# Performance work log

Hardware: AMD Instinct MI355X
Metric: run time of the kernel (lower is better)

The kernel has to match this reference:

```python
import jax, jax.numpy as jnp
import numpy as np

H = 12      # heads
P = 4       # dim_point
CHUNK = 256 # chunk_size
DIM_SINGLE = 768
DIM_PAIR = 64
B, N = 1, 1024


def setup_inputs() -> dict:
    key = jax.random.key(0)
    ks = jax.random.split(key, 24)
    s = 0.02
    d = DIM_SINGLE
    inp = {
        'single': jax.random.normal(ks[0], (B, N, d), jnp.float32),
        'pair': jax.random.normal(ks[1], (B, N, N, DIM_PAIR), jnp.float32),
        'rot': jax.random.normal(ks[2], (B, N, 3, 3), jnp.float32),
        'trans': jax.random.normal(ks[3], (B, N, 3), jnp.float32),
        # Linear weights stored as (in, out) so y = x @ W + b
        'Wq': jax.random.normal(ks[4], (d, d), jnp.float32) * s,
        'bq': jnp.zeros((d,), jnp.float32),
        'Wk': jax.random.normal(ks[5], (d, d), jnp.float32) * s,
        'bk': jnp.zeros((d,), jnp.float32),
        'Wv': jax.random.normal(ks[6], (d, d), jnp.float32) * s,
        'bv': jnp.zeros((d,), jnp.float32),
        'Wpb': jax.random.normal(ks[7], (DIM_PAIR, H), jnp.float32) * s,
        'bpb': jnp.zeros((H,), jnp.float32),
        'Wqp': jax.random.normal(ks[8], (d, H * P * 3), jnp.float32) * s,
        'bqp': jnp.zeros((H * P * 3,), jnp.float32),
        'Wkp': jax.random.normal(ks[9], (d, H * P * 3), jnp.float32) * s,
        'bkp': jnp.zeros((H * P * 3,), jnp.float32),
        'Wvp': jax.random.normal(ks[10], (d, H * P * 3), jnp.float32) * s,
        'bvp': jnp.zeros((H * P * 3,), jnp.float32),
        'Wo': jax.random.normal(ks[11], (d, d), jnp.float32) * s,
        'bo': jnp.zeros((d,), jnp.float32),
        'Wpo': jax.random.normal(ks[12], (H * P * 3, d), jnp.float32) * s,
        'bpo': jnp.zeros((d,), jnp.float32),
        'ln_g': jnp.ones((d,), jnp.float32),
        'ln_b': jnp.zeros((d,), jnp.float32),
    }
    return inp


def _layernorm(x, g, b, eps=1e-5):
    mu = jnp.mean(x, axis=-1, keepdims=True)
    var = jnp.mean((x - mu) ** 2, axis=-1, keepdims=True)
    return (x - mu) * jax.lax.rsqrt(var + eps) * g + b


def reference(single, pair, rot, trans, Wq, bq, Wk, bk, Wv, bv, Wpb, bpb,
              Wqp, bqp, Wkp, bkp, Wvp, bvp, Wo, bo, Wpo, bpo, ln_g, ln_b):
    Bs, Ns, C = single.shape
    Ch = C // H
    scale = Ch ** (-0.5)

    q = (single @ Wq + bq).reshape(Bs, Ns, H, Ch)
    k = (single @ Wk + bk).reshape(Bs, Ns, H, Ch)
    v = (single @ Wv + bv).reshape(Bs, Ns, H, Ch)

    # [B,N,N,H] -> [B,H,N,M]
    pair_bias = jnp.transpose(pair @ Wpb + bpb, (0, 3, 1, 2))

    q_pts = (single @ Wqp + bqp).reshape(Bs, Ns, H, P, 3)
    k_pts = (single @ Wkp + bkp).reshape(Bs, Ns, H, P, 3)
    v_pts = (single @ Wvp + bvp).reshape(Bs, Ns, H, P, 3)

    t = trans[:, :, None, None, :]  # [B,N,1,1,3]
    q_pts_g = jnp.einsum('bnhpd,bnde->bnhpe', q_pts, rot) + t
    k_pts_g = jnp.einsum('bnhpd,bnde->bnhpe', k_pts, rot) + t
    v_pts_g = jnp.einsum('bnhpd,bnde->bnhpe', v_pts, rot) + t

    q2_h = jnp.transpose(jnp.sum(q_pts_g ** 2, axis=(3, 4)), (0, 2, 1))  # [B,H,N]
    k2_h = jnp.transpose(jnp.sum(k_pts_g ** 2, axis=(3, 4)), (0, 2, 1))  # [B,H,N]

    scalar_logits = jnp.einsum('bnhc,bmhc->bhnm', q, k) * scale  # [B,H,N,N]

    out_scalar = jnp.zeros((Bs, Ns, H, Ch), single.dtype)
    out_points = jnp.zeros((Bs, Ns, H, P, 3), single.dtype)

    # Faithful to the original: softmax is taken PER CHUNK over the key axis,
    # and the per-chunk weighted sums are accumulated.
    for start in range(0, Ns, CHUNK):
        end = min(start + CHUNK, Ns)
        qk = jnp.einsum('bnhpd,bmhpd->bhnm', q_pts_g, k_pts_g[:, start:end])
        pt_logits = -0.5 * (q2_h[:, :, :, None] + k2_h[:, :, None, start:end]
                            - 2.0 * qk) * scale
        logits = scalar_logits[:, :, :, start:end] + pair_bias[:, :, :, start:end] + pt_logits
        attn = jax.nn.softmax(logits, axis=-1)  # [B,H,N,chunk]
        out_scalar = out_scalar + jnp.einsum('bhnm,bmhc->bnhc', attn, v[:, start:end])
        out_points = out_points + jnp.einsum('bhnm,bmhpd->bnhpd', attn, v_pts_g[:, start:end])

    weighted_scalar = out_scalar.reshape(Bs, Ns, H * Ch)
    weighted_points = out_points.reshape(Bs, Ns, H * P * 3)
    point_proj = weighted_points @ Wpo + bpo
    out = (weighted_scalar + point_proj) @ Wo + bo
    return _layernorm(single + out, ln_g, ln_b)
```

## Files before the change

kernel.cpp:

```cpp
#include <hip/hip_runtime.h>
#include <hip/hip_bf16.h>
#include <stdint.h>

#define NTOK 1024
#define NH 12
#define QPSLAB 2801664

typedef short bf16x8 __attribute__((ext_vector_type(8)));
typedef float f32x4 __attribute__((ext_vector_type(4)));
typedef uint32_t u32x4 __attribute__((ext_vector_type(4)));

__device__ __forceinline__ unsigned short f2bf(float f) {
  union { float f; uint32_t u; } x; x.f = f;
  uint32_t r = x.u + 0x7FFFu + ((x.u >> 16) & 1u);
  return (unsigned short)(r >> 16);
}
__device__ __forceinline__ float bf2f(unsigned short u) {
  union { uint32_t u; float f; } x; x.u = ((uint32_t)u) << 16;
  return x.f;
}
__device__ __forceinline__ bf16x8 pack8(float4 a, float4 b) {
  union { __hip_bfloat162 h2[4]; bf16x8 v; } u;
  u.h2[0] = __float22bfloat162_rn(make_float2(a.x, a.y));
  u.h2[1] = __float22bfloat162_rn(make_float2(a.z, a.w));
  u.h2[2] = __float22bfloat162_rn(make_float2(b.x, b.y));
  u.h2[3] = __float22bfloat162_rn(make_float2(b.z, b.w));
  return u.v;
}

__global__ __launch_bounds__(256) void prep_k(
    const float* __restrict__ single, const float* __restrict__ Wq,
    const float* __restrict__ Wk, const float* __restrict__ Wv,
    const float* __restrict__ Wqp, const float* __restrict__ Wkp,
    const float* __restrict__ Wvp, const float* __restrict__ Wpo,
    const float* __restrict__ Wo, const float* __restrict__ Wpb,
    const float* __restrict__ bq, const float* __restrict__ bk,
    const float* __restrict__ bv, const float* __restrict__ bqp,
    const float* __restrict__ bkp, const float* __restrict__ bvp,
    unsigned short* __restrict__ sgl, unsigned short* __restrict__ wcat,
    unsigned short* __restrict__ WB, unsigned short* __restrict__ wpoA,
    float* __restrict__ bcat, unsigned short* __restrict__ wpbt)
{
  const int bid = blockIdx.x, t = threadIdx.x;
  if (bid < 2628) {
    __shared__ unsigned short tl[16][72];
    int b = bid;
    const float* src; unsigned short* dst; int N, dstld, rowbase;
    if (b < 1728) {
      int j = b / 576; b -= j * 576;
      src = (j == 0) ? Wq : (j == 1) ? Wk : Wv;
      N = 768; dst = wcat; dstld = 768; rowbase = j * 768;
    } else if (b < 2052) {
      b -= 1728; int j = b / 108; b -= j * 108;
      src = (j == 0) ? Wqp : (j == 1) ? Wkp : Wvp;
      N = 144; dst = wcat; dstld = 768; rowbase = 2304 + j * 144;
    } else {
      b -= 2052; src = Wo; N = 768; dst = WB; dstld = 912; rowbase = 0;
    }
    const int k0 = (b % 12) * 64, n0 = (b / 12) * 16;
#pragma unroll
    for (int i = 0; i < 4; ++i) {
      int kk = (t >> 4) + i * 16;
      int nn = t & 15;
      tl[nn][kk] = f2bf(src[(size_t)(k0 + kk) * N + n0 + nn]);
    }
    __syncthreads();
#pragma unroll
    for (int i = 0; i < 4; ++i) {
      int kk = t & 63;
      int nn = (t >> 6) + i * 4;
      dst[(size_t)(rowbase + n0 + nn) * dstld + k0 + kk] = tl[nn][kk];
    }
    return;
  }
  if (bid < 3396) {
    int i = (bid - 2628) * 256 + t;
    float4 v = *(const float4*)(single + (size_t)i * 4);
    ushort4 o;
    o.x = f2bf(v.x); o.y = f2bf(v.y); o.z = f2bf(v.z); o.w = f2bf(v.w);
    *(ushort4*)(sgl + (size_t)i * 4) = o;
    return;
  }
  if (bid < 3504) {
    int i = (bid - 3396) * 256 + t;
    float4 v = *(const float4*)(Wpo + (size_t)i * 4);
    ushort4 o;
    o.x = f2bf(v.x); o.y = f2bf(v.y); o.z = f2bf(v.z); o.w = f2bf(v.w);
    *(ushort4*)(wpoA + (size_t)i * 4) = o;
    return;
  }
  if (bid < 3515) {
    int idx = (bid - 3504) * 256 + t;
    if (idx < 2736) {
      float v;
      if (idx < 768) v = bq[idx];
      else if (idx < 1536) v = bk[idx - 768];
      else if (idx < 2304) v = bv[idx - 1536];
      else if (idx < 2448) v = bqp[idx - 2304];
      else if (idx < 2592) v = bkp[idx - 2448];
      else v = bvp[idx - 2592];
      bcat[idx] = v;
    }
    return;
  }
  {
    int idx = (bid - 3515) * 256 + t;
    int h = idx >> 6, k = idx & 63;
    wpbt[idx] = (h < 12) ? f2bf(Wpb[k * 12 + h]) : (unsigned short)0;
  }
}

template <int EPI>
__device__ __forceinline__ void gemm_dev(
    unsigned short* As, unsigned short* Bs,
    const unsigned short* __restrict__ A, int lda, int Mact,
    const unsigned short* __restrict__ Bt, int ldb, int Nact,
    int kt0, int ktn, int kmax,
    float* __restrict__ outf, unsigned short* __restrict__ outb, int ldc,
    const float* __restrict__ p0, int mb, int nb, int addbias)
{
  const int t = threadIdx.x;
  const int w = t >> 6, lane = t & 63;
  const int wr = w >> 1, wc = w & 1;
  const int lr = lane & 15, lc = lane >> 4;
  const int m0 = mb * 128, n0 = nb * 128;
  const int r0 = t >> 2, c0 = t & 3;
  const int r1 = r0 + 64;

  f32x4 acc[4][4] = {};
  u32x4 zz = {0u, 0u, 0u, 0u};
  u32x4 pa0, pa1, pq0, pq1;

#define LOAD_AB(KT)                                                              \
  do {                                                                           \
    int k0_ = (KT) * 32;                                                         \
    int g0_ = k0_ + c0 * 8;                                                      \
    pa0 = (g0_ < kmax && (m0 + r0) < Mact)                                       \
              ? *(const u32x4*)(A + (size_t)(m0 + r0) * lda + g0_) : zz;         \
    pa1 = (g0_ < kmax && (m0 + r1) < Mact)                                       \
              ? *(const u32x4*)(A + (size_t)(m0 + r1) * lda + g0_) : zz;         \
    pq0 = (g0_ < kmax && (n0 + r0) < Nact)                                       \
              ? *(const u32x4*)(Bt + (size_t)(n0 + r0) * ldb + g0_) : zz;        \
    pq1 = (g0_ < kmax && (n0 + r1) < Nact)                                       \
              ? *(const u32x4*)(Bt + (size_t)(n0 + r1) * ldb + g0_) : zz;        \
  } while (0)

  LOAD_AB(kt0);
  for (int kt = kt0; kt < kt0 + ktn; ++kt) {
    __syncthreads();
    ((u32x4*)As)[r0 * 4 + c0] = pa0;
    ((u32x4*)As)[r1 * 4 + c0] = pa1;
    ((u32x4*)Bs)[r0 * 4 + c0] = pq0;
    ((u32x4*)Bs)[r1 * 4 + c0] = pq1;
    __syncthreads();
    if (kt + 1 < kt0 + ktn) LOAD_AB(kt + 1);

    bf16x8 af[4], bfr[4];
#pragma unroll
    for (int mi = 0; mi < 4; ++mi) {
      int row = wr * 64 + mi * 16 + lr;
      af[mi] = *(const bf16x8*)(As + (row * 4 + lc) * 8);
    }
#pragma unroll
    for (int ni = 0; ni < 4; ++ni) {
      int row = wc * 64 + ni * 16 + lr;
      bfr[ni] = *(const bf16x8*)(Bs + (row * 4 + lc) * 8);
    }
#pragma unroll
    for (int mi = 0; mi < 4; ++mi)
#pragma unroll
      for (int ni = 0; ni < 4; ++ni)
        acc[mi][ni] = __builtin_amdgcn_mfma_f32_16x16x32_bf16(
            af[mi], bfr[ni], acc[mi][ni], 0, 0, 0);
  }
#undef LOAD_AB

#pragma unroll
  for (int mi = 0; mi < 4; ++mi) {
#pragma unroll
    for (int ni = 0; ni < 4; ++ni) {
#pragma unroll
      for (int r = 0; r < 4; ++r) {
        int row = m0 + wr * 64 + mi * 16 + lc * 4 + r;
        int col = n0 + wc * 64 + ni * 16 + lr;
        if (row < Mact && col < Nact) {
          float v = acc[mi][ni][r];
          if constexpr (EPI == 0) {
            outf[(size_t)row * ldc + col] = addbias ? (v + p0[col]) : v;
          } else {
            outb[(size_t)col * 912 + 768 + row] = f2bf(v);
          }
        }
      }
    }
  }
}

__global__ __launch_bounds__(256) void fat_k(
    const unsigned short* __restrict__ sgl, const unsigned short* __restrict__ wcat,
    const float* __restrict__ bcat, float* __restrict__ qp2,
    const float* __restrict__ pair, const unsigned short* __restrict__ wpbt,
    const float* __restrict__ bpb, unsigned short* __restrict__ pb,
    const unsigned short* __restrict__ wpoA, unsigned short* __restrict__ WB,
    const float* __restrict__ bpo, const float* __restrict__ Wo,
    const float* __restrict__ bo, float* __restrict__ bfused)
{
  const int bid = blockIdx.x;
  const int t = threadIdx.x;

  if (bid < 4096) {
    const int w = t >> 6, lane = t & 63;
    const int lr = lane & 15, g = lane >> 4;
    bf16x8 wf0 = *(const bf16x8*)(wpbt + lr * 64 + g * 8);
    bf16x8 wf1 = *(const bf16x8*)(wpbt + lr * 64 + 32 + g * 8);
    const float bias_h = (lr < 12) ? bpb[lr] : 0.f;
    const int wid = bid * 4 + w;
    const float* s = pair + ((size_t)(wid * 64) + lr) * 64 + g * 8;
    float4 nA = *(const float4*)(s);
    float4 nB = *(const float4*)(s + 4);
    float4 nC = *(const float4*)(s + 32);
    float4 nD = *(const float4*)(s + 36);
#pragma unroll
    for (int it = 0; it < 4; ++it) {
      float4 aA = nA, aB = nB, aC = nC, aD = nD;
      if (it < 3) {
        const float* p = s + (size_t)(it + 1) * 1024;
        nA = *(const float4*)(p);
        nB = *(const float4*)(p + 4);
        nC = *(const float4*)(p + 32);
        nD = *(const float4*)(p + 36);
      }
      bf16x8 f0 = pack8(aA, aB);
      bf16x8 f1 = pack8(aC, aD);
      f32x4 c = {0.f, 0.f, 0.f, 0.f};
      c = __builtin_amdgcn_mfma_f32_16x16x32_bf16(f0, wf0, c, 0, 0, 0);
      c = __builtin_amdgcn_mfma_f32_16x16x32_bf16(f1, wf1, c, 0, 0, 0);
      if (lr < 12) {
        int nm0 = (wid * 4 + it) * 16;
        union { __hip_bfloat162 h2[2]; ushort4 s4; } pu;
        pu.h2[0] = __float22bfloat162_rn(make_float2(c[0] + bias_h, c[1] + bias_h));
        pu.h2[1] = __float22bfloat162_rn(make_float2(c[2] + bias_h, c[3] + bias_h));
        *(ushort4*)(pb + ((size_t)lr << 20) + (size_t)nm0 + g * 4) = pu.s4;
      }
    }
    return;
  }

  __shared__ unsigned short As[128 * 32];
  __shared__ unsigned short Bs[128 * 32];
  int rb = bid - 4096;
  if (rb < 12) {
    int mb = rb & 1, nb = rb >> 1;
    gemm_dev<1>(As, Bs, wpoA, 768, 144, WB, 912, 768, 0, 24, 768,
                nullptr, WB, 912, nullptr, mb, nb, 0);
    return;
  }
  if (rb < 15) {
    int n = (rb - 12) * 256 + t;
    float sacc = bo[n];
    for (int j = 0; j < 768; ++j) sacc += bpo[j] * Wo[(size_t)j * 768 + n];
    bfused[n] = sacc;
    return;
  }
  {
    int pbid = rb - 15;
    int zk = pbid / 176, rem = pbid % 176;
    int mb = rem & 7, nb = rem >> 3;
    gemm_dev<0>(As, Bs, sgl, 768, 1024, wcat, 768, 2736,
                zk * 12, 12, 768,
                qp2 + (size_t)zk * QPSLAB, nullptr, 2736, bcat, mb, nb, zk == 0);
  }
}

__global__ __launch_bounds__(256) void rotate_k(
    const float* __restrict__ qp2, const float* __restrict__ rot,
    const float* __restrict__ trans,
    unsigned short* __restrict__ Acat, unsigned short* __restrict__ Bcat,
    unsigned short* __restrict__ VcatT, float* __restrict__ q2k2)
{
  const int n = blockIdx.x, t = threadIdx.x;
  __shared__ float R[9], T[3], rg[432];
  if (t < 9) R[t] = rot[n * 9 + t];
  if (t >= 9 && t < 12) T[t - 9] = trans[n * 3 + (t - 9)];
  __syncthreads();
  for (int s = t; s < 432; s += 256) {
    int j = s / 144, r = s % 144;
    int h = r / 12, wo = r % 12;
    int e = wo % 3;
    size_t base = (size_t)n * 2736 + 2304 + j * 144 + (r - e);
    float d0 = qp2[base + 0] + qp2[base + 0 + QPSLAB];
    float d1 = qp2[base + 1] + qp2[base + 1 + QPSLAB];
    float d2 = qp2[base + 2] + qp2[base + 2 + QPSLAB];
    float val = d0 * R[e] + d1 * R[3 + e] + d2 * R[6 + e] + T[e];
    rg[s] = val;
    unsigned short bv = f2bf(val);
    if (j == 0)      Acat[((size_t)h * NTOK + n) * 96 + 64 + wo] = bv;
    else if (j == 1) Bcat[((size_t)h * NTOK + n) * 96 + 64 + wo] = bv;
    else             VcatT[((size_t)h * 80 + 64 + wo) * NTOK + n] = bv;
  }
  __syncthreads();
  for (int s = t; s < 2304; s += 256) {
    int j = s / 768, c = s % 768;
    int h = c >> 6, cc = c & 63;
    size_t ix = (size_t)n * 2736 + s;
    unsigned short bv = f2bf(qp2[ix] + qp2[ix + QPSLAB]);
    if (j == 0)      Acat[((size_t)h * NTOK + n) * 96 + cc] = bv;
    else if (j == 1) Bcat[((size_t)h * NTOK + n) * 96 + cc] = bv;
    else             VcatT[((size_t)h * 80 + cc) * NTOK + n] = bv;
  }
  if (t < 240) {
    int h = t / 20, ix = 76 + t % 20;
    Acat[((size_t)h * NTOK + n) * 96 + ix] = 0;
    Bcat[((size_t)h * NTOK + n) * 96 + ix] = 0;
  }
  if (t >= 240 && t < 288) {
    int s = t - 240;
    int h = s / 4, rr = 76 + s % 4;
    VcatT[((size_t)h * 80 + rr) * NTOK + n] = 0;
  }
  if (t < 24) {
    int j = t / 12, h = t % 12;
    float sum = 0.f;
#pragma unroll
    for (int wo = 0; wo < 12; ++wo) {
      float v = rg[j * 144 + h * 12 + wo];
      sum += v * v;
    }
    q2k2[(size_t)(j * NH + h) * NTOK + n] = sum;
  }
}

__global__ __launch_bounds__(256) void attn_k(
    const unsigned short* __restrict__ pb, const unsigned short* __restrict__ Acat,
    const unsigned short* __restrict__ Bcat, const unsigned short* __restrict__ VcatT,
    const float* __restrict__ q2k2, float* __restrict__ acc4)
{
  __shared__ unsigned short Ls[64 * 256];
  __shared__ unsigned short Bs[128 * 104];
  const int t = threadIdx.x, w = t >> 6, lane = t & 63;
  const int lr = lane & 15, lc = lane >> 4;
  const int n0 = blockIdx.x * 64;
  const int m0 = blockIdx.y * 256;
  const int h  = blockIdx.z;

  const unsigned short* Pg = pb + ((size_t)h << 20) + (size_t)n0 * 1024 + m0;
#pragma unroll
  for (int i = 0; i < 8; ++i) {
    int idx = i * 256 + t;
    int row = idx >> 5, sl = idx & 31;
    u32x4 v = *(const u32x4*)(Pg + (size_t)row * 1024 + sl * 8);
    ((u32x4*)Ls)[row * 32 + (sl ^ (row & 7))] = v;
  }
  const unsigned short* Kg = Bcat + ((size_t)h * 1024 + m0) * 96;
#pragma unroll
  for (int i = 0; i < 6; ++i) {
    int idx = i * 256 + t;
    int row = idx / 12, c = idx % 12;
    u32x4 v = *(const u32x4*)(Kg + (size_t)row * 96 + c * 8);
    *(u32x4*)(Bs + row * 104 + c * 8) = v;
  }
  __syncthreads();

  bf16x8 qf[3];
  const unsigned short* Qg = Acat + ((size_t)h * 1024 + n0 + w * 16 + lr) * 96;
#pragma unroll
  for (int kk = 0; kk < 3; ++kk) qf[kk] = *(const bf16x8*)(Qg + kk * 32 + lc * 8);

  f32x4 sa[16];
#pragma unroll
  for (int ct = 0; ct < 16; ++ct) sa[ct] = (f32x4){0.f, 0.f, 0.f, 0.f};

#pragma unroll
  for (int ct = 0; ct < 8; ++ct)
#pragma unroll
    for (int kk = 0; kk < 3; ++kk) {
      bf16x8 kf = *(const bf16x8*)(Bs + (ct * 16 + lr) * 104 + kk * 32 + lc * 8);
      sa[ct] = __builtin_amdgcn_mfma_f32_16x16x32_bf16(kf, qf[kk], sa[ct], 0, 0, 0);
    }
  __syncthreads();
#pragma unroll
  for (int i = 0; i < 6; ++i) {
    int idx = i * 256 + t;
    int row = idx / 12, c = idx % 12;
    u32x4 v = *(const u32x4*)(Kg + (size_t)(128 + row) * 96 + c * 8);
    *(u32x4*)(Bs + row * 104 + c * 8) = v;
  }
  __syncthreads();
#pragma unroll
  for (int ct = 8; ct < 16; ++ct)
#pragma unroll
    for (int kk = 0; kk < 3; ++kk) {
      bf16x8 kf = *(const bf16x8*)(Bs + ((ct - 8) * 16 + lr) * 104 + kk * 32 + lc * 8);
      sa[ct] = __builtin_amdgcn_mfma_f32_16x16x32_bf16(kf, qf[kk], sa[ct], 0, 0, 0);
    }

  const int nrow = w * 16 + lr;
  const float q2v = q2k2[(size_t)h * 1024 + n0 + nrow];
  const float* k2b = q2k2 + 12288 + (size_t)h * 1024 + m0;
  float mx = -1e30f;
#pragma unroll
  for (int ct = 0; ct < 16; ++ct) {
    int sl = (ct * 2 + (lc >> 1)) ^ (nrow & 7);
    const unsigned short* p = Ls + nrow * 256 + sl * 8 + (lc & 1) * 4;
    ushort4 pv = *(const ushort4*)p;
    float4 k2v = *(const float4*)(k2b + ct * 16 + lc * 4);
    sa[ct][0] = 0.125f * sa[ct][0] + bf2f(pv.x) - 0.0625f * (q2v + k2v.x);
    sa[ct][1] = 0.125f * sa[ct][1] + bf2f(pv.y) - 0.0625f * (q2v + k2v.y);
    sa[ct][2] = 0.125f * sa[ct][2] + bf2f(pv.z) - 0.0625f * (q2v + k2v.z);
    sa[ct][3] = 0.125f * sa[ct][3] + bf2f(pv.w) - 0.0625f * (q2v + k2v.w);
    mx = fmaxf(mx, fmaxf(fmaxf(sa[ct][0], sa[ct][1]), fmaxf(sa[ct][2], sa[ct][3])));
  }
  mx = fmaxf(mx, __shfl_xor(mx, 16, 64));
  mx = fmaxf(mx, __shfl_xor(mx, 32, 64));
  float sm = 0.f;
#pragma unroll
  for (int ct = 0; ct < 16; ++ct)
#pragma unroll
    for (int r = 0; r < 4; ++r) { sa[ct][r] = __expf(sa[ct][r] - mx); sm += sa[ct][r]; }
  sm += __shfl_xor(sm, 16, 64);
  sm += __shfl_xor(sm, 32, 64);
  float inv = 1.0f / sm;
#pragma unroll
  for (int ct = 0; ct < 16; ++ct) {
    int sl = (ct * 2 + (lc >> 1)) ^ (nrow & 7);
    unsigned short* p = Ls + nrow * 256 + sl * 8 + (lc & 1) * 4;
    union { __hip_bfloat162 h2[2]; ushort4 s4; } pu;
    pu.h2[0] = __float22bfloat162_rn(make_float2(sa[ct][0] * inv, sa[ct][1] * inv));
    pu.h2[1] = __float22bfloat162_rn(make_float2(sa[ct][2] * inv, sa[ct][3] * inv));
    *(ushort4*)p = pu.s4;
  }
  __syncthreads();

  f32x4 acc[5];
#pragma unroll
  for (int nf = 0; nf < 5; ++nf) acc[nf] = (f32x4){0.f, 0.f, 0.f, 0.f};
  const unsigned short* Vg = VcatT + (size_t)h * 80 * NTOK + m0;
#pragma unroll
  for (int kk = 0; kk < 8; ++kk) {
    int row = w * 16 + lr;
    int sl = (kk * 4 + lc) ^ (row & 7);
    bf16x8 a = *(const bf16x8*)(Ls + row * 256 + sl * 8);
#pragma unroll
    for (int nf = 0; nf < 5; ++nf) {
      int c = nf * 16 + lr;
      bf16x8 b = *(const bf16x8*)(Vg + (size_t)c * NTOK + kk * 32 + lc * 8);
      acc[nf] = __builtin_amdgcn_mfma_f32_16x16x32_bf16(a, b, acc[nf], 0, 0, 0);
    }
  }
  float* out = acc4 + ((size_t)blockIdx.y * NH + h) * (size_t)NTOK * 80;
#pragma unroll
  for (int nf = 0; nf < 5; ++nf)
#pragma unroll
    for (int r = 0; r < 4; ++r) {
      int orow = n0 + w * 16 + lc * 4 + r;
      int c = nf * 16 + lr;
      out[(size_t)orow * 80 + c] = acc[nf][r];
    }
}

__global__ __launch_bounds__(256) void reduce_k(
    const float* __restrict__ acc4, unsigned short* __restrict__ AW)
{
  int idx = blockIdx.x * 256 + threadIdx.x;
  if (idx >= 1024 * 912) return;
  int n = idx / 912, c = idx % 912;
  const size_t cs = (size_t)NH * NTOK * 80;
  size_t base;
  if (c < 768) {
    int h = c >> 6, cc = c & 63;
    base = ((size_t)h * NTOK + n) * 80 + cc;
  } else {
    int c2 = c - 768;
    int h = c2 / 12, wo = c2 % 12;
    base = ((size_t)h * NTOK + n) * 80 + 64 + wo;
  }
  float v = acc4[base] + acc4[base + cs] + acc4[base + 2 * cs] + acc4[base + 3 * cs];
  AW[(size_t)n * 912 + c] = f2bf(v);
}

__global__ __launch_bounds__(256) void tail_gemm_k(
    const unsigned short* __restrict__ AW, const unsigned short* __restrict__ WB,
    float* __restrict__ outpre)
{
  __shared__ unsigned short As[128 * 32];
  __shared__ unsigned short Bs[128 * 32];
  int z = blockIdx.z;
  int kt0 = z * 8, ktn = (z < 3) ? 8 : 5;
  gemm_dev<0>(As, Bs, AW, 912, 1024, WB, 912, 768, kt0, ktn, 912,
              outpre + (size_t)z * 786432, nullptr, 768, nullptr,
              blockIdx.x, blockIdx.y, 0);
}

__global__ __launch_bounds__(256) void ln_k(
    const float* __restrict__ single, const float* __restrict__ outpre,
    const float* __restrict__ bfused, const float* __restrict__ g,
    const float* __restrict__ b, float* __restrict__ out)
{
  const int row = blockIdx.x, t = threadIdx.x;
  __shared__ float red[8];
  size_t base = (size_t)row * 768;
  const size_t SL = 786432;
  float x[3];
#pragma unroll
  for (int j = 0; j < 3; ++j) {
    int c = t + j * 256;
    float v = single[base + c] + bfused[c];
#pragma unroll
    for (int z = 0; z < 4; ++z) v += outpre[base + c + (size_t)z * SL];
    x[j] = v;
  }
  float s = x[0] + x[1] + x[2];
#pragma unroll
  for (int off = 32; off; off >>= 1) s += __shfl_xor(s, off, 64);
  if ((t & 63) == 0) red[t >> 6] = s;
  __syncthreads();
  float mu = (red[0] + red[1] + red[2] + red[3]) * (1.0f / 768.0f);
  float d0 = x[0] - mu, d1 = x[1] - mu, d2 = x[2] - mu;
  float vs = d0 * d0 + d1 * d1 + d2 * d2;
#pragma unroll
  for (int off = 32; off; off >>= 1) vs += __shfl_xor(vs, off, 64);
  if ((t & 63) == 0) red[4 + (t >> 6)] = vs;
  __syncthreads();
  float var = (red[4] + red[5] + red[6] + red[7]) * (1.0f / 768.0f);
  float rs = rsqrtf(var + 1e-5f);
  out[base + t]       = d0 * rs * g[t]       + b[t];
  out[base + t + 256] = d1 * rs * g[t + 256] + b[t + 256];
  out[base + t + 512] = d2 * rs * g[t + 512] + b[t + 512];
}

extern "C" void kernel_launch(void* const* d_in, const int* in_sizes, int n_in,
                              void* d_out, int out_size, void* d_ws, size_t ws_size,
                              hipStream_t stream)
{
  (void)in_sizes; (void)n_in; (void)out_size; (void)ws_size;
  const float* single = (const float*)d_in[0];
  const float* pair   = (const float*)d_in[1];
  const float* rot    = (const float*)d_in[2];
  const float* trans  = (const float*)d_in[3];
  const float* Wq  = (const float*)d_in[4];  const float* bq  = (const float*)d_in[5];
  const float* Wk  = (const float*)d_in[6];  const float* bk  = (const float*)d_in[7];
  const float* Wv  = (const float*)d_in[8];  const float* bv  = (const float*)d_in[9];
  const float* Wpb = (const float*)d_in[10]; const float* bpb = (const float*)d_in[11];
  const float* Wqp = (const float*)d_in[12]; const float* bqp = (const float*)d_in[13];
  const float* Wkp = (const float*)d_in[14]; const float* bkp = (const float*)d_in[15];
  const float* Wvp = (const float*)d_in[16]; const float* bvp = (const float*)d_in[17];
  const float* Wo  = (const float*)d_in[18]; const float* bo  = (const float*)d_in[19];
  const float* Wpo = (const float*)d_in[20]; const float* bpo = (const float*)d_in[21];
  const float* lng = (const float*)d_in[22]; const float* lnb = (const float*)d_in[23];

  char* ws = (char*)d_ws;
  unsigned short* sgl    = (unsigned short*)(ws + 0);
  unsigned short* wcat   = (unsigned short*)(ws + 1572864);
  unsigned short* wpoA   = (unsigned short*)(ws + 5775360);
  unsigned short* WB     = (unsigned short*)(ws + 5996544);
  float*          bcat   = (float*)(ws + 7397376);
  unsigned short* wpbt   = (unsigned short*)(ws + 7408320);
  float*          bfused = (float*)(ws + 7410432);
  float*          qp2    = (float*)(ws + 7413504);
  unsigned short* Acat   = (unsigned short*)(ws + 29826816);
  unsigned short* Bcat   = (unsigned short*)(ws + 32186112);
  unsigned short* VcatT  = (unsigned short*)(ws + 34545408);
  float*          q2k2   = (float*)(ws + 36511488);
  unsigned short* pb     = (unsigned short*)(ws + 36609792);
  float*          acc4   = (float*)(ws + 61775616);
  unsigned short* AW     = (unsigned short*)(ws + 77504256);
  float*          outpre = (float*)(ws + 79372032);

  prep_k<<<3519, 256, 0, stream>>>(single, Wq, Wk, Wv, Wqp, Wkp, Wvp, Wpo, Wo,
                                   Wpb, bq, bk, bv, bqp, bkp, bvp,
                                   sgl, wcat, WB, wpoA, bcat, wpbt);

  fat_k<<<4463, 256, 0, stream>>>(sgl, wcat, bcat, qp2, pair, wpbt, bpb, pb,
                                  wpoA, WB, bpo, Wo, bo, bfused);

  rotate_k<<<1024, 256, 0, stream>>>(qp2, rot, trans, Acat, Bcat, VcatT, q2k2);

  attn_k<<<dim3(16, 4, 12), 256, 0, stream>>>(pb, Acat, Bcat, VcatT, q2k2, acc4);

  reduce_k<<<3648, 256, 0, stream>>>(acc4, AW);

  tail_gemm_k<<<dim3(8, 6, 4), 256, 0, stream>>>(AW, WB, outpre);

  ln_k<<<1024, 256, 0, stream>>>(single, outpre, bfused, lng, lnb, (float*)d_out);
}
```

Baseline: 192.1 us.

## Coalesce pair-bias loads via LDS staging and schedule GEMM blocks first

The pair-bias projection in fat_k now reads the fp32 pair tensor with fully contiguous per-lane float4 loads. It converts them to bf16 and stages them in double-buffered shared memory, then reads them back in the MFMA fragment layout. Before, each lane loaded strided 32-byte pieces directly. Block ordering is also swapped so the GEMM and bias-fusion blocks get the low block indices and launch before the many pair-bias blocks. The cost is a block-wide __syncthreads per iteration and extra LDS traffic, and the larger shared allocation may reduce occupancy.

After: 166.2 us. 1.16x faster.

```diff
diff --git a/kernel.cpp b/kernel.cpp
--- a/kernel.cpp
+++ b/kernel.cpp
@@ -18,14 +18,6 @@
 __device__ __forceinline__ float bf2f(unsigned short u) {
   union { uint32_t u; float f; } x; x.u = ((uint32_t)u) << 16;
   return x.f;
-}
-__device__ __forceinline__ bf16x8 pack8(float4 a, float4 b) {
-  union { __hip_bfloat162 h2[4]; bf16x8 v; } u;
-  u.h2[0] = __float22bfloat162_rn(make_float2(a.x, a.y));
-  u.h2[1] = __float22bfloat162_rn(make_float2(a.z, a.w));
-  u.h2[2] = __float22bfloat162_rn(make_float2(b.x, b.y));
-  u.h2[3] = __float22bfloat162_rn(make_float2(b.z, b.w));
-  return u.v;
 }
 
 __global__ __launch_bounds__(256) void prep_k(
@@ -205,36 +197,81 @@
     const float* __restrict__ bpo, const float* __restrict__ Wo,
     const float* __restrict__ bo, float* __restrict__ bfused)
 {
+  __shared__ unsigned short shmem[8704];
   const int bid = blockIdx.x;
   const int t = threadIdx.x;
 
-  if (bid < 4096) {
-    const int w = t >> 6, lane = t & 63;
+  if (bid < 12) {
+    int mb = bid & 1, nb = bid >> 1;
+    gemm_dev<1>(shmem, shmem + 4096, wpoA, 768, 144, WB, 912, 768, 0, 24, 768,
+                nullptr, WB, 912, nullptr, mb, nb, 0);
+    return;
+  }
+  if (bid < 15) {
+    int n = (bid - 12) * 256 + t;
+    float sacc = bo[n];
+    for (int j = 0; j < 768; ++j) sacc += bpo[j] * Wo[(size_t)j * 768 + n];
+    bfused[n] = sacc;
+    return;
+  }
+  if (bid < 367) {
+    int pbid = bid - 15;
+    int zk = pbid / 176, rem = pbid % 176;
+    int mb = rem & 7, nb = rem >> 3;
+    gemm_dev<0>(shmem, shmem + 4096, sgl, 768, 1024, wcat, 768, 2736,
+                zk * 12, 12, 768,
+                qp2 + (size_t)zk * QPSLAB, nullptr, 2736, bcat, mb, nb, zk == 0);
+    return;
+  }
+  {
+    const int lane = t & 63, w = t >> 6;
     const int lr = lane & 15, g = lane >> 4;
+    unsigned short* b0 = shmem + (w * 2 + 0) * 1088;
+    unsigned short* b1 = shmem + (w * 2 + 1) * 1088;
     bf16x8 wf0 = *(const bf16x8*)(wpbt + lr * 64 + g * 8);
     bf16x8 wf1 = *(const bf16x8*)(wpbt + lr * 64 + 32 + g * 8);
     const float bias_h = (lr < 12) ? bpb[lr] : 0.f;
-    const int wid = bid * 4 + w;
-    const float* s = pair + ((size_t)(wid * 64) + lr) * 64 + g * 8;
-    float4 nA = *(const float4*)(s);
-    float4 nB = *(const float4*)(s + 4);
-    float4 nC = *(const float4*)(s + 32);
-    float4 nD = *(const float4*)(s + 36);
+    const int wid = (bid - 367) * 4 + w;
+    const float* base = pair + (size_t)wid * 4096;
+
+#define PB_WR(BUF, I, V)                                                         \
+    do {                                                                         \
+      union { __hip_bfloat162 h2[2]; ushort4 s4; } u_;                           \
+      u_.h2[0] = __float22bfloat162_rn(make_float2((V).x, (V).y));               \
+      u_.h2[1] = __float22bfloat162_rn(make_float2((V).z, (V).w));               \
+      *(ushort4*)((BUF) + ((I) * 4 + g) * 68 + lr * 4) = u_.s4;                  \
+    } while (0)
+
+    {
+      float4 v0 = *(const float4*)(base + 0 * 256 + lane * 4);
+      float4 v1 = *(const float4*)(base + 1 * 256 + lane * 4);
+      float4 v2 = *(const float4*)(base + 2 * 256 + lane * 4);
+      float4 v3 = *(const float4*)(base + 3 * 256 + lane * 4);
+      PB_WR(b0, 0, v0); PB_WR(b0, 1, v1); PB_WR(b0, 2, v2); PB_WR(b0, 3, v3);
+    }
 #pragma unroll
     for (int it = 0; it < 4; ++it) {
-      float4 aA = nA, aB = nB, aC = nC, aD = nD;
+      unsigned short* cur = (it & 1) ? b1 : b0;
+      unsigned short* nxt = (it & 1) ? b0 : b1;
+      float4 n0, n1, n2, n3;
       if (it < 3) {
-        const float* p = s + (size_t)(it + 1) * 1024;
-        nA = *(const float4*)(p);
-        nB = *(const float4*)(p + 4);
-        nC = *(const float4*)(p + 32);
-        nD = *(const float4*)(p + 36);
+        const float* p = base + (it + 1) * 1024;
+        n0 = *(const float4*)(p + 0 * 256 + lane * 4);
+        n1 = *(const float4*)(p + 1 * 256 + lane * 4);
+        n2 = *(const float4*)(p + 2 * 256 + lane * 4);
+        n3 = *(const float4*)(p + 3 * 256 + lane * 4);
       }
-      bf16x8 f0 = pack8(aA, aB);
-      bf16x8 f1 = pack8(aC, aD);
+      __syncthreads();
+      union { ushort4 q[2]; bf16x8 v; } F0, F1;
+      F0.q[0] = *(const ushort4*)(cur + lr * 68 + g * 8);
+      F0.q[1] = *(const ushort4*)(cur + lr * 68 + g * 8 + 4);
+      F1.q[0] = *(const ushort4*)(cur + lr * 68 + 32 + g * 8);
+      F1.q[1] = *(const ushort4*)(cur + lr * 68 + 32 + g * 8 + 4);
+      if (it < 3) { PB_WR(nxt, 0, n0); PB_WR(nxt, 1, n1);
+                    PB_WR(nxt, 2, n2); PB_WR(nxt, 3, n3); }
       f32x4 c = {0.f, 0.f, 0.f, 0.f};
-      c = __builtin_amdgcn_mfma_f32_16x16x32_bf16(f0, wf0, c, 0, 0, 0);
-      c = __builtin_amdgcn_mfma_f32_16x16x32_bf16(f1, wf1, c, 0, 0, 0);
+      c = __builtin_amdgcn_mfma_f32_16x16x32_bf16(F0.v, wf0, c, 0, 0, 0);
+      c = __builtin_amdgcn_mfma_f32_16x16x32_bf16(F1.v, wf1, c, 0, 0, 0);
       if (lr < 12) {
         int nm0 = (wid * 4 + it) * 16;
         union { __hip_bfloat162 h2[2]; ushort4 s4; } pu;
@@ -243,32 +280,7 @@
         *(ushort4*)(pb + ((size_t)lr << 20) + (size_t)nm0 + g * 4) = pu.s4;
       }
     }
-    return;
-  }
-
-  __shared__ unsigned short As[128 * 32];
-  __shared__ unsigned short Bs[128 * 32];
-  int rb = bid - 4096;
-  if (rb < 12) {
-    int mb = rb & 1, nb = rb >> 1;
-    gemm_dev<1>(As, Bs, wpoA, 768, 144, WB, 912, 768, 0, 24, 768,
-                nullptr, WB, 912, nullptr, mb, nb, 0);
-    return;
-  }
-  if (rb < 15) {
-    int n = (rb - 12) * 256 + t;
-    float sacc = bo[n];
-    for (int j = 0; j < 768; ++j) sacc += bpo[j] * Wo[(size_t)j * 768 + n];
-    bfused[n] = sacc;
-    return;
-  }
-  {
-    int pbid = rb - 15;
-    int zk = pbid / 176, rem = pbid % 176;
-    int mb = rem & 7, nb = rem >> 3;
-    gemm_dev<0>(As, Bs, sgl, 768, 1024, wcat, 768, 2736,
-                zk * 12, 12, 768,
-                qp2 + (size_t)zk * QPSLAB, nullptr, 2736, bcat, mb, nb, zk == 0);
+#undef PB_WR
   }
 }
 
```
